# Kernel optimization log

Measured on AMD Instinct MI355X. Metric: run time of the kernel, lower is better.

## Reference

```python
import jax, jax.numpy as jnp
import numpy as np
import math
from jax.scipy.special import gammaln, logsumexp

N, D, K = 262144, 16, 64
K_TRUE = 32
TAU = 0.1
LOG2PI = math.log(2.0 * math.pi)


def setup_inputs() -> dict:
    key = jax.random.key(0)
    k0, k1, k2, k3, k4, k5 = jax.random.split(key, 6)
    # data locations, scaled so log(r_scale_met) > 0 (Gamma rate positivity, as in original init)
    met_locs = jax.random.normal(k0, (N, D), dtype=jnp.float32) * 20.0
    R = met_locs.max(0) - met_locs.min(0)  # per-dim range, diag of Ro
    r_scale = jnp.sqrt(jnp.sum(R ** 2)) / (2.0 * K_TRUE)
    mu = jax.random.normal(k1, (K, D), dtype=jnp.float32) * jnp.sqrt(R)[None, :]  # MVN(0, Ro)
    pi = jax.random.dirichlet(k2, jnp.full((K,), 1.0 / K, dtype=jnp.float32)).astype(jnp.float32)
    # log of Gamma(0.5, rate=0.5) sample; clipped for numerical safety of the setup draw
    lambda_mu = jnp.clip(jnp.log(jax.random.gamma(k3, 0.5, (D,)) / 0.5), -3.0, 3.0).astype(jnp.float32)
    b = jax.random.normal(k4, (K, D), dtype=jnp.float32)
    C = jnp.full((K,), jnp.log(r_scale), dtype=jnp.float32)
    r = jnp.full((K,), jnp.log(r_scale), dtype=jnp.float32)
    z = jax.random.normal(k5, (N, K), dtype=jnp.float32)
    return {"met_locs": met_locs, "mu": mu, "pi": pi, "lambda_mu": lambda_mu,
            "b": b, "C": C, "r": r, "z": z}


def reference(met_locs, mu, pi, lambda_mu, b, C, r, z):
    Df = float(D)
    R = met_locs.max(0) - met_locs.min(0)                      # diag of Ro
    c = 1.25 + (D - 1) / 4.0
    g = 0.25 + (D - 1) / 4.0
    G = c / (50.0 * g) * jnp.sqrt(jnp.sum(R ** 2))

    # ---- z_loss: Concrete prior on z_act + Concrete-weighted Gaussian mixture ----
    logz = jax.nn.log_softmax(z, axis=1)                       # log z_act, [N, K]
    logpi = jax.nn.log_softmax(pi)                             # [K]
    # isotropic Gaussian log N(x_m; mu_k, exp(r_k) I) without [N,K,D] intermediate
    sq = ((met_locs ** 2).sum(1, keepdims=True)
          - 2.0 * met_locs @ mu.T
          + (mu ** 2).sum(1)[None, :])                          # [N, K]
    logN = -0.5 * sq / jnp.exp(r)[None, :] - 0.5 * Df * (r + LOG2PI)[None, :]
    mix = logsumexp(logz + logN, axis=1)                       # log sum_k z_mk N_k(x_m)
    # Concrete (Gumbel-softmax) log-density at y = z_act with probs softmax(pi), temp TAU
    t = logpi[None, :] - TAU * logz                            # [N, K]
    con = (gammaln(float(K)) + (K - 1) * math.log(TAU)
           + jnp.sum(logpi) - (TAU + 1.0) * logz.sum(1)
           - K * logsumexp(t, axis=1))                          # [N]
    z_loss = -(con + mix).sum()

    # ---- pi_loss: Dirichlet(1/K) prior (up to const) ----
    pi_loss = -((1.0 / K - 1.0) * logpi).sum()

    # ---- mu_loss: MVN(b, Lambda Ro Lambda) with Lambda = diag(lambda_mu) ----
    var_mu = (lambda_mu ** 2) * R                              # diag of Bo, [D]
    mu_lp = (-0.5 * (((mu - b) ** 2) / var_mu[None, :]).sum(1)
             - 0.5 * jnp.log(var_mu).sum() - 0.5 * Df * LOG2PI)
    mu_loss = -mu_lp.sum()

    # ---- lambda_loss: Gamma(0.5, 0.5) on exp(lambda_mu) ----
    lam_lp = (0.5 * math.log(0.5) - gammaln(0.5)
              + (0.5 - 1.0) * lambda_mu - 0.5 * jnp.exp(lambda_mu))
    lambda_loss = -lam_lp.sum()

    # ---- b_loss: standard normal MVN ----
    b_loss = 0.5 * (b ** 2).sum() + 0.5 * K * Df * LOG2PI

    # ---- r_loss: Gamma(c, rate=C) on 1/exp(r) ----
    r_lp = c * jnp.log(C) + (c - 1.0) * (-r) - C * jnp.exp(-r) - gammaln(c)
    r_loss = -r_lp.sum()

    # ---- C_loss: Gamma(g, rate=G) on 1/exp(C) ----
    C_lp = g * jnp.log(G) + (g - 1.0) * (-C) - G * jnp.exp(-C) - gammaln(g)
    C_loss = -C_lp.sum()

    # forward sums in self.learn order: r, mu, z, pi, b, lambda, C
    return r_loss + mu_loss + z_loss + pi_loss + b_loss + lambda_loss + C_loss
```

## Files before the change

kernel.cpp:

```cpp
#include <hip/hip_runtime.h>
#include <math.h>

#define NROWS   262144
#define NBLK    2048
#define NTHR    256
#define NWAVES  (NBLK*NTHR/64)
#define NITER   (NROWS/NWAVES)
#define LOG2PI_F 1.8378770664093453f

template<int CTRL>
__device__ __forceinline__ float dppf(float x){
  return __int_as_float(__builtin_amdgcn_update_dpp(
      0, __float_as_int(x), CTRL, 0xF, 0xF, true));
}
__device__ __forceinline__ float rl63(float x){
  return __int_as_float(__builtin_amdgcn_readlane(__float_as_int(x), 63));
}
__device__ __forceinline__ float wsum(float x){
  x += dppf<0x111>(x); x += dppf<0x112>(x); x += dppf<0x114>(x); x += dppf<0x118>(x);
  x += dppf<0x142>(x); x += dppf<0x143>(x);
  return rl63(x);
}
__device__ __forceinline__ float wmax(float x){
  x = fmaxf(x, dppf<0x111>(x)); x = fmaxf(x, dppf<0x112>(x));
  x = fmaxf(x, dppf<0x114>(x)); x = fmaxf(x, dppf<0x118>(x));
  x = fmaxf(x, dppf<0x142>(x)); x = fmaxf(x, dppf<0x143>(x));
  return rl63(x);
}

__global__ __launch_bounds__(NTHR, 8)
void zloss_main(const float* __restrict__ met, const float* __restrict__ mu,
                const float* __restrict__ pi,  const float* __restrict__ rr,
                const float* __restrict__ z,   float* __restrict__ ws)
{
  float* wacc = ws;
  float* wzs  = ws + NBLK;
  float* wmn  = ws + 2*NBLK;
  float* wmx  = wmn + NBLK*16;

  __shared__ float s_acc[4], s_zs[4], s_mn[4][16], s_mx[4][16];

  const int tid  = threadIdx.x;
  const int lane = tid & 63;
  const int wid  = tid >> 6;
  const int k    = lane;

  float pik = pi[k];
  float rk  = rr[k];
  float mrow[16];
  #pragma unroll
  for (int d=0; d<16; ++d) mrow[d] = mu[k*16+d];
  float lse_pi = __logf(wsum(__expf(pik)));
  float lpk = pik - lse_pi;
  float ir  = __expf(-rk);
  float mumu = 0.f;
  #pragma unroll
  for (int d=0; d<16; ++d) mumu = fmaf(mrow[d], mrow[d], mumu);
  float Bk = -0.5f*ir;
  float Dk = fmaf(Bk, mumu, -8.0f*(rk + LOG2PI_F));
  float r0 = __int_as_float(__builtin_amdgcn_readlane(__float_as_int(rk), 0));
  const int runi = __all(rk == r0);

  int n = __builtin_amdgcn_readfirstlane((int)(blockIdx.x*blockDim.x + (unsigned)tid) >> 6);
  float zk = z[(size_t)n*64 + k];
  float xl = met[(size_t)n*16 + (k & 15)];

  float accA=0.f, zsA=0.f, xqA=0.f;
  float mn = INFINITY, mx = -INFINITY;

  #pragma unroll 1
  for (int it=0; it<NITER; ++it){
    int nn = (it < NITER-1) ? (n + NWAVES) : n;
    float zk_n = z[(size_t)nn*64 + k];
    float xl_n = met[(size_t)nn*16 + (k & 15)];
    const float4* rp = (const float4*)(met + (size_t)n*16);
    float4 a = rp[0], b = rp[1], c = rp[2], e = rp[3];

    float ez = __expf(zk);
    float eu = __expf(fmaf(-0.1f, zk, lpk));
    mn = fminf(mn, xl); mx = fmaxf(mx, xl);
    zsA += zk;

    float dot = 0.f;
    dot = fmaf(a.x, mrow[0],  dot); dot = fmaf(a.y, mrow[1],  dot);
    dot = fmaf(a.z, mrow[2],  dot); dot = fmaf(a.w, mrow[3],  dot);
    dot = fmaf(b.x, mrow[4],  dot); dot = fmaf(b.y, mrow[5],  dot);
    dot = fmaf(b.z, mrow[6],  dot); dot = fmaf(b.w, mrow[7],  dot);
    dot = fmaf(c.x, mrow[8],  dot); dot = fmaf(c.y, mrow[9],  dot);
    dot = fmaf(c.z, mrow[10], dot); dot = fmaf(c.w, mrow[11], dot);
    dot = fmaf(e.x, mrow[12], dot); dot = fmaf(e.y, mrow[13], dot);
    dot = fmaf(e.z, mrow[14], dot); dot = fmaf(e.w, mrow[15], dot);
    float av = zk + fmaf(ir, dot, Dk);
    if (runi){
      xqA = fmaf(xl, xl, xqA);
    } else {
      float xx = 0.f;
      xx = fmaf(a.x,a.x,xx); xx = fmaf(a.y,a.y,xx); xx = fmaf(a.z,a.z,xx); xx = fmaf(a.w,a.w,xx);
      xx = fmaf(b.x,b.x,xx); xx = fmaf(b.y,b.y,xx); xx = fmaf(b.z,b.z,xx); xx = fmaf(b.w,b.w,xx);
      xx = fmaf(c.x,c.x,xx); xx = fmaf(c.y,c.y,xx); xx = fmaf(c.z,c.z,xx); xx = fmaf(c.w,c.w,xx);
      xx = fmaf(e.x,e.x,xx); xx = fmaf(e.y,e.y,xx); xx = fmaf(e.z,e.z,xx); xx = fmaf(e.w,e.w,xx);
      av = fmaf(Bk, xx, av);
    }

    float sez = wsum(ez);
    float seu = wsum(eu);
    float ma  = wmax(av);
    float ea  = __expf(av - ma);
    float sea = wsum(ea);
    float lse_z = __logf(sez);
    float rowv = fmaf(63.f, lse_z, ma) + __logf(sea) - 64.f*__logf(seu);
    accA += rowv;

    n = nn; zk = zk_n; xl = xl_n;
  }

  if (runi) accA = fmaf(Bk, wsum(xqA)*0.25f, accA);
  float zsW = wsum(zsA);

  mn = fminf(mn, __shfl_xor(mn, 16)); mn = fminf(mn, __shfl_xor(mn, 32));
  mx = fmaxf(mx, __shfl_xor(mx, 16)); mx = fmaxf(mx, __shfl_xor(mx, 32));

  if (lane == 0){ s_acc[wid] = accA; s_zs[wid] = zsW; }
  if (lane < 16){ s_mn[wid][lane] = mn; s_mx[wid][lane] = mx; }
  __syncthreads();
  if (tid == 0){
    wacc[blockIdx.x] = s_acc[0]+s_acc[1]+s_acc[2]+s_acc[3];
    wzs [blockIdx.x] = s_zs[0]+s_zs[1]+s_zs[2]+s_zs[3];
  }
  if (tid < 16){
    wmn[blockIdx.x*16+tid] = fminf(fminf(s_mn[0][tid],s_mn[1][tid]),fminf(s_mn[2][tid],s_mn[3][tid]));
    wmx[blockIdx.x*16+tid] = fmaxf(fmaxf(s_mx[0][tid],s_mx[1][tid]),fmaxf(s_mx[2][tid],s_mx[3][tid]));
  }
}

__global__ __launch_bounds__(NTHR)
void finalize(const float* __restrict__ mu, const float* __restrict__ pi,
              const float* __restrict__ lam, const float* __restrict__ bp,
              const float* __restrict__ Cv,  const float* __restrict__ rr,
              const float* __restrict__ ws,  float* __restrict__ out,
              float cgam, float lamconst, float lg_c, float lg_g)
{
  const float* wacc = ws;
  const float* wzs  = ws + NBLK;
  const float* wmn  = ws + 2*NBLK;
  const float* wmx  = wmn + NBLK*16;

  __shared__ double sda[NTHR], sdz[NTHR];
  __shared__ float rmn[16][16], rmx[16][16];
  __shared__ float Rfin[16], vars[16];

  const int tid = threadIdx.x;

  double da = 0.0, dz = 0.0;
  for (int b2 = tid; b2 < NBLK; b2 += NTHR){ da += (double)wacc[b2]; dz += (double)wzs[b2]; }
  sda[tid] = da; sdz[tid] = dz;
  __syncthreads();
  for (int s = NTHR/2; s > 0; s >>= 1){
    if (tid < s){ sda[tid] += sda[tid+s]; sdz[tid] += sdz[tid+s]; }
    __syncthreads();
  }

  {
    int d = tid & 15, g = tid >> 4;
    float mng = INFINITY, mxg = -INFINITY;
    for (int j = 0; j < NBLK/16; ++j){
      int b2 = g + 16*j;
      mng = fminf(mng, wmn[b2*16+d]);
      mxg = fmaxf(mxg, wmx[b2*16+d]);
    }
    rmn[g][d] = mng; rmx[g][d] = mxg;
  }
  __syncthreads();
  if (tid < 16){
    float mnv = rmn[0][tid], mxv = rmx[0][tid];
    #pragma unroll
    for (int g = 1; g < 16; ++g){ mnv = fminf(mnv, rmn[g][tid]); mxv = fmaxf(mxv, rmx[g][tid]); }
    float Rd = mxv - mnv;
    Rfin[tid] = Rd;
    float l = lam[tid];
    vars[tid] = l*l*Rd;
  }
  __syncthreads();

  if (tid < 64){
    int kk = tid;
    float sumR2 = 0.f;
    #pragma unroll
    for (int dd = 0; dd < 16; ++dd) sumR2 = fmaf(Rfin[dd], Rfin[dd], sumR2);
    float G = 0.025f * sqrtf(sumR2);

    float pik2 = pi[kk];
    float sp   = wsum(pik2);
    float lse2 = __logf(wsum(__expf(pik2)));
    float slogpi = sp - 64.f*lse2;

    float qsum = 0.f, slv = 0.f, bb = 0.f;
    #pragma unroll
    for (int dd = 0; dd < 16; ++dd){
      float df = mu[kk*16+dd] - bp[kk*16+dd];
      qsum += df*df / vars[dd];
      slv  += __logf(vars[dd]);
      float bv = bp[kk*16+dd];
      bb = fmaf(bv, bv, bb);
    }
    float mu_term = 0.5f*qsum + 0.5f*slv + 8.0f*LOG2PI_F;
    float rk2 = rr[kk], Ck = Cv[kk];
    float r_lp = 5.f*__logf(Ck) - 4.f*rk2 - Ck*__expf(-rk2) - lg_c;
    float C_lp = 4.f*__logf(G)  - 3.f*Ck  - G*__expf(-Ck)  - lg_g;
    float lam_term = 0.f;
    if (kk < 16){ float l = lam[kk]; lam_term = lamconst - 0.5f*l - 0.5f*__expf(l); }

    float per = mu_term + 0.5f*bb - r_lp - C_lp - lam_term;
    float persum = wsum(per);

    if (kk == 0){
      double zpart = sda[0] + 262144.0*(double)(cgam + slogpi) - 1.1*sdz[0];
      double tot = (double)persum
                 + (1.0 - 1.0/64.0)*(double)slogpi
                 + 512.0*(double)LOG2PI_F
                 - zpart;
      out[0] = (float)tot;
    }
  }
}

extern "C" void kernel_launch(void* const* d_in, const int* in_sizes, int n_in,
                              void* d_out, int out_size, void* d_ws, size_t ws_size,
                              hipStream_t stream) {
  const float* met = (const float*)d_in[0];
  const float* mu  = (const float*)d_in[1];
  const float* pi  = (const float*)d_in[2];
  const float* lam = (const float*)d_in[3];
  const float* bpp = (const float*)d_in[4];
  const float* Cv  = (const float*)d_in[5];
  const float* rr  = (const float*)d_in[6];
  const float* zz  = (const float*)d_in[7];
  float* out = (float*)d_out;
  float* ws  = (float*)d_ws;

  float cgam     = (float)(lgamma(64.0) + 63.0*log(0.1));
  float lamconst = (float)(0.5*log(0.5) - lgamma(0.5));
  float lg_c     = (float)lgamma(5.0);
  float lg_g     = (float)lgamma(4.0);

  zloss_main<<<dim3(NBLK), dim3(NTHR), 0, stream>>>(met, mu, pi, rr, zz, ws);
  finalize<<<dim3(1), dim3(NTHR), 0, stream>>>(mu, pi, lam, bpp, Cv, rr, ws, out,
                                               cgam, lamconst, lg_c, lg_g);
}
```

Baseline: 162.6 us.

## Switch to row-per-lane layout with online logsumexp and LDS-transposed z

Moves from one-wave-per-row (each lane a component k, reduced across lanes with DPP) to one-lane-per-row: each lane loops over all 64 components with an online logsumexp, reading z through a padded LDS transpose and mu/constants as wave-uniform loads. Per-component constants move into a separate setup kernel. exp/log use base-2 hardware intrinsics. Min/max of met are computed with coalesced float4 loads, and the block count is halved. The intent is to drop the per-row cross-lane reductions and the redundant row loads, at the cost of an extra kernel launch and more LDS use.

Result: faster. 131.5 us (-19.1%).

```diff
diff --git a/kernel.cpp b/kernel.cpp
--- a/kernel.cpp
+++ b/kernel.cpp
@@ -1,17 +1,24 @@
 #include <hip/hip_runtime.h>
 #include <math.h>
 
-#define NROWS   262144
-#define NBLK    2048
-#define NTHR    256
-#define NWAVES  (NBLK*NTHR/64)
-#define NITER   (NROWS/NWAVES)
+#define NROWS 262144
+#define NBLK  1024
+#define NTHR  256
 #define LOG2PI_F 1.8378770664093453f
+#define L2E_F   1.4426950408889634f
+#define LN2_F   0.6931471805599453f
+
+#define EXP2F(x) __builtin_amdgcn_exp2f(x)
+#define LOG2F(x) __builtin_amdgcn_logf(x)
+
+#define WS_ZS   1024
+#define WS_MN   2048
+#define WS_MX   18432
+#define WS_CONS 34816
 
 template<int CTRL>
 __device__ __forceinline__ float dppf(float x){
-  return __int_as_float(__builtin_amdgcn_update_dpp(
-      0, __float_as_int(x), CTRL, 0xF, 0xF, true));
+  return __int_as_float(__builtin_amdgcn_update_dpp(0, __float_as_int(x), CTRL, 0xF, 0xF, true));
 }
 __device__ __forceinline__ float rl63(float x){
   return __int_as_float(__builtin_amdgcn_readlane(__float_as_int(x), 63));
@@ -21,160 +28,186 @@
   x += dppf<0x142>(x); x += dppf<0x143>(x);
   return rl63(x);
 }
-__device__ __forceinline__ float wmax(float x){
-  x = fmaxf(x, dppf<0x111>(x)); x = fmaxf(x, dppf<0x112>(x));
-  x = fmaxf(x, dppf<0x114>(x)); x = fmaxf(x, dppf<0x118>(x));
-  x = fmaxf(x, dppf<0x142>(x)); x = fmaxf(x, dppf<0x143>(x));
-  return rl63(x);
-}
-
-__global__ __launch_bounds__(NTHR, 8)
-void zloss_main(const float* __restrict__ met, const float* __restrict__ mu,
-                const float* __restrict__ pi,  const float* __restrict__ rr,
-                const float* __restrict__ z,   float* __restrict__ ws)
-{
-  float* wacc = ws;
-  float* wzs  = ws + NBLK;
-  float* wmn  = ws + 2*NBLK;
-  float* wmx  = wmn + NBLK*16;
-
-  __shared__ float s_acc[4], s_zs[4], s_mn[4][16], s_mx[4][16];
-
-  const int tid  = threadIdx.x;
-  const int lane = tid & 63;
-  const int wid  = tid >> 6;
-  const int k    = lane;
-
-  float pik = pi[k];
-  float rk  = rr[k];
-  float mrow[16];
-  #pragma unroll
-  for (int d=0; d<16; ++d) mrow[d] = mu[k*16+d];
+
+__global__ void setup_k(const float* __restrict__ mu, const float* __restrict__ pi,
+                        const float* __restrict__ rr, float* __restrict__ ws){
+  int k = threadIdx.x;
+  float pik = pi[k], rk = rr[k];
+  float mumu = 0.f;
+  #pragma unroll
+  for (int d = 0; d < 16; ++d){ float m = mu[k*16+d]; mumu = fmaf(m, m, mumu); }
   float lse_pi = __logf(wsum(__expf(pik)));
   float lpk = pik - lse_pi;
-  float ir  = __expf(-rk);
-  float mumu = 0.f;
-  #pragma unroll
-  for (int d=0; d<16; ++d) mumu = fmaf(mrow[d], mrow[d], mumu);
-  float Bk = -0.5f*ir;
-  float Dk = fmaf(Bk, mumu, -8.0f*(rk + LOG2PI_F));
-  float r0 = __int_as_float(__builtin_amdgcn_readlane(__float_as_int(rk), 0));
-  const int runi = __all(rk == r0);
-
-  int n = __builtin_amdgcn_readfirstlane((int)(blockIdx.x*blockDim.x + (unsigned)tid) >> 6);
-  float zk = z[(size_t)n*64 + k];
-  float xl = met[(size_t)n*16 + (k & 15)];
-
-  float accA=0.f, zsA=0.f, xqA=0.f;
-  float mn = INFINITY, mx = -INFINITY;
-
-  #pragma unroll 1
-  for (int it=0; it<NITER; ++it){
-    int nn = (it < NITER-1) ? (n + NWAVES) : n;
-    float zk_n = z[(size_t)nn*64 + k];
-    float xl_n = met[(size_t)nn*16 + (k & 15)];
-    const float4* rp = (const float4*)(met + (size_t)n*16);
-    float4 a = rp[0], b = rp[1], c = rp[2], e = rp[3];
-
-    float ez = __expf(zk);
-    float eu = __expf(fmaf(-0.1f, zk, lpk));
-    mn = fminf(mn, xl); mx = fmaxf(mx, xl);
-    zsA += zk;
-
-    float dot = 0.f;
-    dot = fmaf(a.x, mrow[0],  dot); dot = fmaf(a.y, mrow[1],  dot);
-    dot = fmaf(a.z, mrow[2],  dot); dot = fmaf(a.w, mrow[3],  dot);
-    dot = fmaf(b.x, mrow[4],  dot); dot = fmaf(b.y, mrow[5],  dot);
-    dot = fmaf(b.z, mrow[6],  dot); dot = fmaf(b.w, mrow[7],  dot);
-    dot = fmaf(c.x, mrow[8],  dot); dot = fmaf(c.y, mrow[9],  dot);
-    dot = fmaf(c.z, mrow[10], dot); dot = fmaf(c.w, mrow[11], dot);
-    dot = fmaf(e.x, mrow[12], dot); dot = fmaf(e.y, mrow[13], dot);
-    dot = fmaf(e.z, mrow[14], dot); dot = fmaf(e.w, mrow[15], dot);
-    float av = zk + fmaf(ir, dot, Dk);
-    if (runi){
-      xqA = fmaf(xl, xl, xqA);
-    } else {
-      float xx = 0.f;
-      xx = fmaf(a.x,a.x,xx); xx = fmaf(a.y,a.y,xx); xx = fmaf(a.z,a.z,xx); xx = fmaf(a.w,a.w,xx);
-      xx = fmaf(b.x,b.x,xx); xx = fmaf(b.y,b.y,xx); xx = fmaf(b.z,b.z,xx); xx = fmaf(b.w,b.w,xx);
-      xx = fmaf(c.x,c.x,xx); xx = fmaf(c.y,c.y,xx); xx = fmaf(c.z,c.z,xx); xx = fmaf(c.w,c.w,xx);
-      xx = fmaf(e.x,e.x,xx); xx = fmaf(e.y,e.y,xx); xx = fmaf(e.z,e.z,xx); xx = fmaf(e.w,e.w,xx);
-      av = fmaf(Bk, xx, av);
-    }
-
-    float sez = wsum(ez);
-    float seu = wsum(eu);
-    float ma  = wmax(av);
-    float ea  = __expf(av - ma);
-    float sea = wsum(ea);
-    float lse_z = __logf(sez);
-    float rowv = fmaf(63.f, lse_z, ma) + __logf(sea) - 64.f*__logf(seu);
-    accA += rowv;
-
-    n = nn; zk = zk_n; xl = xl_n;
-  }
-
-  if (runi) accA = fmaf(Bk, wsum(xqA)*0.25f, accA);
-  float zsW = wsum(zsA);
-
-  mn = fminf(mn, __shfl_xor(mn, 16)); mn = fminf(mn, __shfl_xor(mn, 32));
-  mx = fmaxf(mx, __shfl_xor(mx, 16)); mx = fmaxf(mx, __shfl_xor(mx, 32));
-
-  if (lane == 0){ s_acc[wid] = accA; s_zs[wid] = zsW; }
-  if (lane < 16){ s_mn[wid][lane] = mn; s_mx[wid][lane] = mx; }
+  float ir = __expf(-rk), Bk = -0.5f*ir;
+  float Dk = fmaf(Bk, mumu, -8.f*(rk + LOG2PI_F));
+  float* cons = ws + WS_CONS;
+  cons[k*4+0] = __expf(lpk);
+  cons[k*4+1] = ir*L2E_F;
+  cons[k*4+2] = Dk*L2E_F;
+  cons[k*4+3] = Bk*L2E_F;
+}
+
+__global__ __launch_bounds__(NTHR, 4)
+void zmain(const float* __restrict__ met, const float* __restrict__ mu,
+           const float* __restrict__ z, float* __restrict__ ws)
+{
+  __shared__ float zt[4][2112];
+  const int tid = threadIdx.x, lane = tid & 63, wid = tid >> 6;
+  const int bx = blockIdx.x;
+
+  float pmn[4], pmx[4];
+  #pragma unroll
+  for (int j=0;j<4;++j){ pmn[j]=INFINITY; pmx[j]=-INFINITY; }
+  {
+    const float4* mb = (const float4*)(met + (size_t)bx*4096);
+    #pragma unroll
+    for (int i=0;i<4;++i){
+      float4 v = mb[i*256 + tid];
+      pmn[0]=fminf(pmn[0],v.x); pmx[0]=fmaxf(pmx[0],v.x);
+      pmn[1]=fminf(pmn[1],v.y); pmx[1]=fmaxf(pmx[1],v.y);
+      pmn[2]=fminf(pmn[2],v.z); pmx[2]=fmaxf(pmx[2],v.z);
+      pmn[3]=fminf(pmn[3],v.w); pmx[3]=fmaxf(pmx[3],v.w);
+    }
+  }
+
+  const int rbw = bx*256 + wid*64;
+  const float4* xr = (const float4*)(met + (size_t)(rbw + lane)*16);
+  float4 xa = xr[0], xb = xr[1], xc = xr[2], xd = xr[3];
+  float xx = 0.f;
+  xx=fmaf(xa.x,xa.x,xx); xx=fmaf(xa.y,xa.y,xx); xx=fmaf(xa.z,xa.z,xx); xx=fmaf(xa.w,xa.w,xx);
+  xx=fmaf(xb.x,xb.x,xx); xx=fmaf(xb.y,xb.y,xx); xx=fmaf(xb.z,xb.z,xx); xx=fmaf(xb.w,xb.w,xx);
+  xx=fmaf(xc.x,xc.x,xx); xx=fmaf(xc.y,xc.y,xx); xx=fmaf(xc.z,xc.z,xx); xx=fmaf(xc.w,xc.w,xx);
+  xx=fmaf(xd.x,xd.x,xx); xx=fmaf(xd.y,xd.y,xx); xx=fmaf(xd.z,xd.z,xx); xx=fmaf(xd.w,xd.w,xx);
+
+  const float4* z4 = (const float4*)z;
+  const int g8 = lane >> 3, c8 = lane & 7;
+  float4 sA[8], sB[8];
+  #pragma unroll
+  for (int j=0;j<8;++j) sA[j] = z4[(size_t)(rbw + j*8 + g8)*16 + c8];
+  #pragma unroll
+  for (int j=0;j<8;++j) sB[j] = z4[(size_t)(rbw + j*8 + g8)*16 + 8 + c8];
+  #pragma unroll
+  for (int j=0;j<8;++j){
+    int b = (j*8+g8)*33 + c8*4;
+    zt[wid][b]=sA[j].x; zt[wid][b+1]=sA[j].y; zt[wid][b+2]=sA[j].z; zt[wid][b+3]=sA[j].w;
+  }
+
+  const float4* cons4 = (const float4*)(ws + WS_CONS);
+  const float4* mu4   = (const float4*)mu;
+
+  float sez=0.f, seu=0.f, sea=0.f, m2=-1e30f, szA=0.f;
+
+#define STEPK(K) { \
+    float4 cc = cons4[K]; \
+    float4 M0 = mu4[(K)*4+0], M1 = mu4[(K)*4+1], M2v = mu4[(K)*4+2], M3 = mu4[(K)*4+3]; \
+    float zkv = zt[wid][lane*33 + ((K)&31)]; \
+    float zk2 = zkv*L2E_F; \
+    szA += zkv; \
+    sez += EXP2F(zk2); \
+    seu = fmaf(cc.x, EXP2F(-0.1f*zk2), seu); \
+    float dt = 0.f; \
+    dt=fmaf(xa.x,M0.x,dt); dt=fmaf(xa.y,M0.y,dt); dt=fmaf(xa.z,M0.z,dt); dt=fmaf(xa.w,M0.w,dt); \
+    dt=fmaf(xb.x,M1.x,dt); dt=fmaf(xb.y,M1.y,dt); dt=fmaf(xb.z,M1.z,dt); dt=fmaf(xb.w,M1.w,dt); \
+    dt=fmaf(xc.x,M2v.x,dt); dt=fmaf(xc.y,M2v.y,dt); dt=fmaf(xc.z,M2v.z,dt); dt=fmaf(xc.w,M2v.w,dt); \
+    dt=fmaf(xd.x,M3.x,dt); dt=fmaf(xd.y,M3.y,dt); dt=fmaf(xd.z,M3.z,dt); dt=fmaf(xd.w,M3.w,dt); \
+    float t1  = fmaf(cc.w, xx, zk2); \
+    float av2 = fmaf(cc.y, dt, t1) + cc.z; \
+    float d2 = av2 - m2; \
+    float ee = EXP2F(-fabsf(d2)); \
+    bool fl = d2 > 0.f; \
+    sea = fmaf(sea, fl?ee:1.f, fl?1.f:ee); \
+    m2 = fmaxf(m2, av2); }
+
+  #pragma unroll 4
+  for (int kk=0; kk<32; ++kk) STEPK(kk)
+
+  #pragma unroll
+  for (int j=0;j<8;++j){
+    int b = (j*8+g8)*33 + c8*4;
+    zt[wid][b]=sB[j].x; zt[wid][b+1]=sB[j].y; zt[wid][b+2]=sB[j].z; zt[wid][b+3]=sB[j].w;
+  }
+  #pragma unroll 4
+  for (int kk=32; kk<64; ++kk) STEPK(kk)
+#undef STEPK
+
+  float l2sez = LOG2F(sez), l2seu = LOG2F(seu), l2sea = LOG2F(sea);
+  float accA = LN2_F * (fmaf(63.f, l2sez, m2 + l2sea) - 64.f*l2seu);
+
+  __syncthreads();
+  float* scr = &zt[0][0];
+  float wa = wsum(accA), wz = wsum(szA);
+  if (lane == 0){ scr[2112 + wid] = wa; scr[2120 + wid] = wz; }
+  #pragma unroll
+  for (int j=0;j<4;++j){
+    int d = (4*tid + j) & 15;
+    scr[       d*66 + (tid>>2)] = pmn[j];
+    scr[1056 + d*66 + (tid>>2)] = pmx[j];
+  }
   __syncthreads();
   if (tid == 0){
-    wacc[blockIdx.x] = s_acc[0]+s_acc[1]+s_acc[2]+s_acc[3];
-    wzs [blockIdx.x] = s_zs[0]+s_zs[1]+s_zs[2]+s_zs[3];
+    ws[bx]         = scr[2112]+scr[2113]+scr[2114]+scr[2115];
+    ws[WS_ZS + bx] = scr[2120]+scr[2121]+scr[2122]+scr[2123];
   }
   if (tid < 16){
-    wmn[blockIdx.x*16+tid] = fminf(fminf(s_mn[0][tid],s_mn[1][tid]),fminf(s_mn[2][tid],s_mn[3][tid]));
-    wmx[blockIdx.x*16+tid] = fmaxf(fmaxf(s_mx[0][tid],s_mx[1][tid]),fmaxf(s_mx[2][tid],s_mx[3][tid]));
+    float mnv = INFINITY, mxv = -INFINITY;
+    for (int c2=0;c2<64;++c2){
+      mnv = fminf(mnv, scr[tid*66+c2]);
+      mxv = fmaxf(mxv, scr[1056+tid*66+c2]);
+    }
+    ws[WS_MN + bx*16 + tid] = mnv;
+    ws[WS_MX + bx*16 + tid] = mxv;
   }
 }
 
 __global__ __launch_bounds__(NTHR)
-void finalize(const float* __restrict__ mu, const float* __restrict__ pi,
-              const float* __restrict__ lam, const float* __restrict__ bp,
-              const float* __restrict__ Cv,  const float* __restrict__ rr,
-              const float* __restrict__ ws,  float* __restrict__ out,
-              float cgam, float lamconst, float lg_c, float lg_g)
+void fin_k(const float* __restrict__ mu, const float* __restrict__ pi,
+           const float* __restrict__ lam, const float* __restrict__ bp,
+           const float* __restrict__ Cv,  const float* __restrict__ rr,
+           const float* __restrict__ ws,  float* __restrict__ out,
+           float cgam, float lamconst, float lg_c, float lg_g)
 {
-  const float* wacc = ws;
-  const float* wzs  = ws + NBLK;
-  const float* wmn  = ws + 2*NBLK;
-  const float* wmx  = wmn + NBLK*16;
-
   __shared__ double sda[NTHR], sdz[NTHR];
-  __shared__ float rmn[16][16], rmx[16][16];
+  __shared__ float smn[16][66], smx[16][66];
   __shared__ float Rfin[16], vars[16];
-
   const int tid = threadIdx.x;
 
-  double da = 0.0, dz = 0.0;
-  for (int b2 = tid; b2 < NBLK; b2 += NTHR){ da += (double)wacc[b2]; dz += (double)wzs[b2]; }
-  sda[tid] = da; sdz[tid] = dz;
+  {
+    const float4* wa4 = (const float4*)ws;
+    const float4* wz4 = (const float4*)(ws + WS_ZS);
+    float4 a = wa4[tid], zz = wz4[tid];
+    sda[tid] = (double)a.x + (double)a.y + (double)a.z + (double)a.w;
+    sdz[tid] = (double)zz.x + (double)zz.y + (double)zz.z + (double)zz.w;
+  }
+  float pmn[4], pmx[4];
+  #pragma unroll
+  for (int j=0;j<4;++j){ pmn[j]=INFINITY; pmx[j]=-INFINITY; }
+  {
+    const float4* mn4 = (const float4*)(ws + WS_MN);
+    const float4* mx4 = (const float4*)(ws + WS_MX);
+    #pragma unroll
+    for (int i=0;i<16;++i){
+      float4 v = mn4[i*256 + tid];
+      pmn[0]=fminf(pmn[0],v.x); pmn[1]=fminf(pmn[1],v.y);
+      pmn[2]=fminf(pmn[2],v.z); pmn[3]=fminf(pmn[3],v.w);
+      float4 w = mx4[i*256 + tid];
+      pmx[0]=fmaxf(pmx[0],w.x); pmx[1]=fmaxf(pmx[1],w.y);
+      pmx[2]=fmaxf(pmx[2],w.z); pmx[3]=fmaxf(pmx[3],w.w);
+    }
+  }
+  #pragma unroll
+  for (int j=0;j<4;++j){
+    int d = (4*tid + j) & 15;
+    smn[d][tid>>2] = pmn[j];
+    smx[d][tid>>2] = pmx[j];
+  }
   __syncthreads();
   for (int s = NTHR/2; s > 0; s >>= 1){
     if (tid < s){ sda[tid] += sda[tid+s]; sdz[tid] += sdz[tid+s]; }
     __syncthreads();
   }
-
-  {
-    int d = tid & 15, g = tid >> 4;
-    float mng = INFINITY, mxg = -INFINITY;
-    for (int j = 0; j < NBLK/16; ++j){
-      int b2 = g + 16*j;
-      mng = fminf(mng, wmn[b2*16+d]);
-      mxg = fmaxf(mxg, wmx[b2*16+d]);
-    }
-    rmn[g][d] = mng; rmx[g][d] = mxg;
-  }
-  __syncthreads();
   if (tid < 16){
-    float mnv = rmn[0][tid], mxv = rmx[0][tid];
-    #pragma unroll
-    for (int g = 1; g < 16; ++g){ mnv = fminf(mnv, rmn[g][tid]); mxv = fmaxf(mxv, rmx[g][tid]); }
+    float mnv = INFINITY, mxv = -INFINITY;
+    for (int c2=0;c2<64;++c2){ mnv = fminf(mnv, smn[tid][c2]); mxv = fmaxf(mxv, smx[tid][c2]); }
     float Rd = mxv - mnv;
     Rfin[tid] = Rd;
     float l = lam[tid];
@@ -243,7 +276,8 @@
   float lg_c     = (float)lgamma(5.0);
   float lg_g     = (float)lgamma(4.0);
 
-  zloss_main<<<dim3(NBLK), dim3(NTHR), 0, stream>>>(met, mu, pi, rr, zz, ws);
-  finalize<<<dim3(1), dim3(NTHR), 0, stream>>>(mu, pi, lam, bpp, Cv, rr, ws, out,
-                                               cgam, lamconst, lg_c, lg_g);
-}
+  setup_k<<<dim3(1), dim3(64), 0, stream>>>(mu, pi, rr, ws);
+  zmain<<<dim3(NBLK), dim3(NTHR), 0, stream>>>(met, mu, zz, ws);
+  fin_k<<<dim3(1), dim3(NTHR), 0, stream>>>(mu, pi, lam, bpp, Cv, rr, ws, out,
+                                            cgam, lamconst, lg_c, lg_g);
+}
```
